# Kernel tuning notes

Measured on AMD Instinct MI355X. Metric: run time of the kernel, lower is better.

The kernel has to match this reference:

```python
import jax, jax.numpy as jnp
import numpy as np
from jax import lax

TOP_K = 2

def setup_inputs() -> dict:
    key = jax.random.key(0)
    ks = jax.random.split(key, 7)
    B, D, H, E = 8192, 1024, 4096, 8
    s = 0.02
    return {
        "x": jax.random.normal(ks[0], (B, D), jnp.float32),
        "wg": jax.random.normal(ks[1], (E, D), jnp.float32) * s,
        "bg": jnp.zeros((E,), jnp.float32),
        "w1": jax.random.normal(ks[2], (E, D, H), jnp.float32) * s,
        "b1": jnp.zeros((E, H), jnp.float32),
        "w2": jax.random.normal(ks[3], (E, H, D), jnp.float32) * s,
        "b2": jnp.zeros((E, D), jnp.float32),
    }

def reference(x, wg, bg, w1, b1, w2, b2):
    # Router: top-k logits, softmax over the selected k logits (TopKGate).
    logits = x @ wg.T + bg                      # (B, E)
    top_vals, top_idx = lax.top_k(logits, TOP_K)  # (B, K)
    gates = jax.nn.softmax(top_vals, axis=-1)     # (B, K)
    # Expert MLPs computed densely for all experts (vectorized reference;
    # dropout is identity in eval mode).
    h = jax.nn.relu(jnp.einsum('bd,edh->ebh', x, w1) + b1[:, None, :])  # (E, B, H)
    all_out = jnp.einsum('ebh,ehd->ebd', h, w2) + b2[:, None, :]        # (E, B, D)
    # Combine: gather each token's top-k expert outputs, weight by gates.
    per_tok = jnp.transpose(all_out, (1, 0, 2))                          # (B, E, D)
    sel = jnp.take_along_axis(per_tok, top_idx[:, :, None], axis=1)      # (B, K, D)
    return jnp.sum(sel * gates[:, :, None], axis=1)                      # (B, D)
```

## Files before the change

kernel.cpp:

```cpp
#include <hip/hip_runtime.h>
#include <hip/hip_bf16.h>
#include <math.h>

#define B_TOK 8192
#define D_DIM 1024
#define H_DIM 4096
#define E_NUM 8
#define NPAIR (B_TOK * 2)

typedef __bf16 bf16x8 __attribute__((ext_vector_type(8)));
typedef float f32x4 __attribute__((ext_vector_type(4)));
typedef unsigned short us4 __attribute__((ext_vector_type(4)));
typedef unsigned short us8 __attribute__((ext_vector_type(8)));

__device__ __forceinline__ unsigned short f2bf(float f) {
  union { float f; unsigned u; } v; v.f = f;
  unsigned r = v.u + 0x7FFFu + ((v.u >> 16) & 1u);
  return (unsigned short)(r >> 16);
}

__device__ __forceinline__ void gload16(const void* g, void* l) {
  __builtin_amdgcn_global_load_lds(
      (const __attribute__((address_space(1))) void*)g,
      (__attribute__((address_space(3))) void*)l, 16, 0, 0);
}

#define BARRIER()    asm volatile("s_barrier" ::: "memory")
#define VM4          asm volatile("s_waitcnt vmcnt(4)" ::: "memory")
#define VM0          asm volatile("s_waitcnt vmcnt(0)" ::: "memory")
#define LGKM0        asm volatile("s_waitcnt lgkmcnt(0)" ::: "memory")
#define RF(x) __builtin_amdgcn_readfirstlane(x)

__global__ void k_prep(const float* __restrict__ x, unsigned short* __restrict__ xb,
                       const float* __restrict__ w1, const float* __restrict__ w2,
                       unsigned short* __restrict__ w1t, unsigned short* __restrict__ w2t,
                       const float* __restrict__ wg, const float* __restrict__ bg,
                       int* __restrict__ tidx, float* __restrict__ tgate) {
  __shared__ unsigned short tl[64][68];
  int b = blockIdx.x;
  int tid = threadIdx.x;
  if (b < 2048) {
    int wid = tid >> 6, lane = tid & 63;
    int tok = b * 4 + wid;
    float acc[E_NUM];
#pragma unroll
    for (int e = 0; e < E_NUM; e++) acc[e] = 0.f;
    const float* xr = x + (size_t)tok * D_DIM;
#pragma unroll
    for (int it = 0; it < D_DIM / 256; it++) {
      int i = it * 256 + lane * 4;
      float4 xv = *(const float4*)(xr + i);
#pragma unroll
      for (int e = 0; e < E_NUM; e++) {
        float4 wv = *(const float4*)(wg + e * D_DIM + i);
        acc[e] += xv.x * wv.x + xv.y * wv.y + xv.z * wv.z + xv.w * wv.w;
      }
    }
#pragma unroll
    for (int e = 0; e < E_NUM; e++) {
#pragma unroll
      for (int off = 32; off; off >>= 1) acc[e] += __shfl_xor(acc[e], off);
    }
    if (lane == 0) {
      float v[E_NUM];
#pragma unroll
      for (int e = 0; e < E_NUM; e++) v[e] = acc[e] + bg[e];
      int i0 = 0; float v0 = v[0];
#pragma unroll
      for (int e = 1; e < E_NUM; e++) if (v[e] > v0) { v0 = v[e]; i0 = e; }
      int i1 = -1; float v1 = -1e30f;
#pragma unroll
      for (int e = 0; e < E_NUM; e++) if (e != i0 && v[e] > v1) { v1 = v[e]; i1 = e; }
      float g0 = 1.f / (1.f + expf(v1 - v0));
      float g1 = 1.f - g0;
      tidx[2 * tok] = i0; tidx[2 * tok + 1] = i1;
      tgate[2 * tok] = g0; tgate[2 * tok + 1] = g1;
    }
  } else if (b < 10240) {
    int i = ((b - 2048) * 256 + tid) * 4;
    float4 v = *(const float4*)(x + i);
    us4 o;
    o[0] = f2bf(v.x); o[1] = f2bf(v.y); o[2] = f2bf(v.z); o[3] = f2bf(v.w);
    *(us4*)(xb + i) = o;
  } else {
    int lb = b - 10240;
    int which = lb >> 13;
    int rem = lb & 8191;
    int e = rem >> 10;
    int local = rem & 1023;
    int R = which ? H_DIM : D_DIM;
    int C = which ? D_DIM : H_DIM;
    int CT = C >> 6;
    int ct = local & (CT - 1);
    int rt = local / CT;
    const float* ine = (which ? w2 : w1) + (size_t)e * D_DIM * H_DIM;
    unsigned short* oute = (which ? w2t : w1t) + (size_t)e * D_DIM * H_DIM;
    int r0 = rt * 64, c0 = ct * 64;
    int c4 = tid & 15, rg = tid >> 4;
    float4 v[4];
#pragma unroll
    for (int it = 0; it < 4; ++it)
      v[it] = *(const float4*)&ine[(size_t)(r0 + rg * 4 + it) * C + c0 + c4 * 4];
#pragma unroll
    for (int j = 0; j < 4; ++j) {
      us4 o;
      o[0] = f2bf(((const float*)&v[0])[j]);
      o[1] = f2bf(((const float*)&v[1])[j]);
      o[2] = f2bf(((const float*)&v[2])[j]);
      o[3] = f2bf(((const float*)&v[3])[j]);
      *(us4*)&tl[c4 * 4 + j][rg * 4] = o;
    }
    __syncthreads();
    int c = tid >> 2, g = tid & 3;
    us4 a0 = *(const us4*)&tl[c][g * 16 + 0];
    us4 a1 = *(const us4*)&tl[c][g * 16 + 4];
    us4 a2 = *(const us4*)&tl[c][g * 16 + 8];
    us4 a3 = *(const us4*)&tl[c][g * 16 + 12];
    us8 o0 = {a0[0], a0[1], a0[2], a0[3], a1[0], a1[1], a1[2], a1[3]};
    us8 o1 = {a2[0], a2[1], a2[2], a2[3], a3[0], a3[1], a3[2], a3[3]};
    size_t obase = (size_t)(c0 + c) * R + r0 + g * 16;
    *(us8*)&oute[obase] = o0;
    *(us8*)&oute[obase + 8] = o1;
  }
}

__global__ void k_count(const int* __restrict__ tidx, int* __restrict__ cnt) {
  __shared__ int lcnt[E_NUM];
  int tid = threadIdx.x;
  if (tid < E_NUM) lcnt[tid] = 0;
  __syncthreads();
  int t = blockIdx.x * 256 + tid;
  atomicAdd(&lcnt[tidx[2 * t]], 1);
  atomicAdd(&lcnt[tidx[2 * t + 1]], 1);
  __syncthreads();
  if (tid < E_NUM) atomicAdd(&cnt[tid], lcnt[tid]);
}

__global__ void k_prefix(int* __restrict__ meta) {
  if (threadIdx.x == 0) {
    int* cnt = meta;
    int* eoff = meta + 8;
    int* cursor = meta + 17;
    int* toff1 = meta + 25;
    int* toff2 = meta + 34;
    int a = 0, t1 = 0, t2 = 0;
    for (int e = 0; e < E_NUM; e++) {
      eoff[e] = a; cursor[e] = a; a += cnt[e];
      toff1[e] = t1; toff2[e] = t2;
      int mc = (cnt[e] + 127) >> 7;
      t1 += mc * (H_DIM / 128);
      t2 += mc * (D_DIM / 128);
    }
    eoff[E_NUM] = a; toff1[E_NUM] = t1; toff2[E_NUM] = t2;
  }
}

__global__ void k_scatter(const int* __restrict__ tidx, const float* __restrict__ tgate,
                          int* __restrict__ cursor, int* __restrict__ ptok,
                          float* __restrict__ pgate) {
  __shared__ int lcnt[E_NUM];
  __shared__ int base[E_NUM];
  int tid = threadIdx.x;
  if (tid < E_NUM) lcnt[tid] = 0;
  __syncthreads();
  int t = blockIdx.x * 256 + tid;
  int e0 = tidx[2 * t], e1 = tidx[2 * t + 1];
  int l0 = atomicAdd(&lcnt[e0], 1);
  int l1 = atomicAdd(&lcnt[e1], 1);
  __syncthreads();
  if (tid < E_NUM) base[tid] = atomicAdd(&cursor[tid], lcnt[tid]);
  __syncthreads();
  int p0 = base[e0] + l0;
  int p1 = base[e1] + l1;
  ptok[p0] = t; pgate[p0] = tgate[2 * t];
  ptok[p1] = t; pgate[p1] = tgate[2 * t + 1];
}

template <int KDIM, int NDIM, int MODE>
__global__ __launch_bounds__(256, 3) void k_gemm(
    const unsigned short* __restrict__ A, const unsigned short* __restrict__ Bt,
    const float* __restrict__ bias, const int* __restrict__ meta,
    const int* __restrict__ ptok, const float* __restrict__ pgate,
    unsigned short* __restrict__ Hout, float* __restrict__ Out) {
  constexpr int NT = NDIM / 128;
  constexpr int NKT = KDIM / 32;
  static_assert(NKT % 3 == 2 && NKT >= 8, "tail pattern requires NKT==2 mod 3");
  const int* eoff = meta + 8;
  const int* toff = (MODE == 1) ? (meta + 25) : (meta + 34);

  int tf[E_NUM + 1];
#pragma unroll
  for (int q = 0; q <= E_NUM; q++) tf[q] = RF(toff[q]);

  int nwg = gridDim.x;
  int bid = blockIdx.x;
  int i = (bid & 7) * (nwg >> 3) + (bid >> 3);
  if (i >= tf[E_NUM]) return;
  int e = 0;
#pragma unroll
  for (int q = 1; q < E_NUM; q++) e += (i >= tf[q]);
  int r = i - tf[e];
  int mt = r / NT;
  int nt = r - mt * NT;
  int off = RF(eoff[e]);
  int cnt = RF(eoff[e + 1]) - off;
  int m0 = mt * 128;

  __shared__ unsigned short lds[3][2][128 * 32];

  int tid = threadIdx.x;
  int w = tid >> 6, lane = tid & 63;
  int wm = w >> 1, wn = w & 1;

  int sseg = (lane & 3) ^ ((lane >> 3) & 3);
  const unsigned short* aSrc[2];
  const unsigned short* bSrc[2];
#pragma unroll
  for (int c = 0; c < 2; c++) {
    int q = w * 2 + c;
    int lrow = q * 16 + (lane >> 2);
    int arow = m0 + lrow;
    int ar = (arow < cnt) ? arow : (cnt - 1);
    size_t grow;
    if (MODE == 1) grow = (size_t)ptok[off + ar];
    else grow = (size_t)(off + ar);
    aSrc[c] = A + grow * KDIM + sseg * 8;
    int nrow = nt * 128 + q * 16 + (lane >> 2);
    bSrc[c] = Bt + (size_t)e * NDIM * KDIM + (size_t)nrow * KDIM + sseg * 8;
  }

  int segp = (lane >> 4) ^ ((lane >> 1) & 3);
  f32x4 acc[4][4] = {};

#define STAGE(buf, k0)                                          \
  {                                                             \
    _Pragma("unroll")                                           \
    for (int c = 0; c < 2; c++) {                               \
      int q = w * 2 + c;                                        \
      gload16(aSrc[c] + (k0), &lds[buf][0][q * 512]);           \
      gload16(bSrc[c] + (k0), &lds[buf][1][q * 512]);           \
    }                                                           \
  }
#define NOSTG ((void)0)

#define STEP(buf, WAITC, STGC)                                              \
  {                                                                         \
    WAITC; BARRIER();                                                       \
    STGC;                                                                   \
    bf16x8 aF[4], bF[4];                                                    \
    _Pragma("unroll")                                                       \
    for (int m = 0; m < 4; m++) {                                           \
      int row = wm * 64 + m * 16 + (lane & 15);                             \
      aF[m] = *(const bf16x8*)&lds[buf][0][row * 32 + segp * 8];            \
    }                                                                       \
    _Pragma("unroll")                                                       \
    for (int n = 0; n < 4; n++) {                                           \
      int row = wn * 64 + n * 16 + (lane & 15);                             \
      bF[n] = *(const bf16x8*)&lds[buf][1][row * 32 + segp * 8];            \
    }                                                                       \
    LGKM0;                                                                  \
    __builtin_amdgcn_s_setprio(1);                                          \
    _Pragma("unroll")                                                       \
    for (int m = 0; m < 4; m++)                                             \
      _Pragma("unroll")                                                     \
      for (int n = 0; n < 4; n++)                                           \
        acc[m][n] =                                                         \
            __builtin_amdgcn_mfma_f32_16x16x32_bf16(aF[m], bF[n], acc[m][n], 0, 0, 0); \
    __builtin_amdgcn_s_setprio(0);                                          \
  }

  STAGE(0, 0);
  STAGE(1, 32);

#pragma unroll 1
  for (int kt = 0; kt < NKT - 5; kt += 3) {
    STEP(0, VM4, STAGE(2, (kt + 2) * 32));
    STEP(1, VM4, STAGE(0, (kt + 3) * 32));
    STEP(2, VM4, STAGE(1, (kt + 4) * 32));
  }
  STEP(0, VM4, STAGE(2, (NKT - 3) * 32));
  STEP(1, VM4, STAGE(0, (NKT - 2) * 32));
  STEP(2, VM4, STAGE(1, (NKT - 1) * 32));
  STEP(0, VM4, NOSTG);
  STEP(1, VM0, NOSTG);

#undef STAGE
#undef NOSTG
#undef STEP

#pragma unroll
  for (int m = 0; m < 4; m++) {
    int lrowb = wm * 64 + m * 16 + (lane >> 4) * 4;
#pragma unroll
    for (int r2 = 0; r2 < 4; r2++) {
      int arow = m0 + lrowb + r2;
      if (arow < cnt) {
        if constexpr (MODE == 1) {
          size_t rowbase = (size_t)(off + arow) * NDIM;
#pragma unroll
          for (int n = 0; n < 4; n++) {
            int col = nt * 128 + wn * 64 + n * 16 + (lane & 15);
            float v = acc[m][n][r2] + bias[e * NDIM + col];
            v = v > 0.f ? v : 0.f;
            Hout[rowbase + col] = f2bf(v);
          }
        } else {
          int tok = ptok[off + arow];
          float g = pgate[off + arow];
#pragma unroll
          for (int n = 0; n < 4; n++) {
            int col = nt * 128 + wn * 64 + n * 16 + (lane & 15);
            float v = (acc[m][n][r2] + bias[e * NDIM + col]) * g;
            atomicAdd(Out + (size_t)tok * D_DIM + col, v);
          }
        }
      }
    }
  }
}

extern "C" void kernel_launch(void* const* d_in, const int* in_sizes, int n_in,
                              void* d_out, int out_size, void* d_ws, size_t ws_size,
                              hipStream_t stream) {
  const float* x  = (const float*)d_in[0];
  const float* wg = (const float*)d_in[1];
  const float* bg = (const float*)d_in[2];
  const float* w1 = (const float*)d_in[3];
  const float* b1 = (const float*)d_in[4];
  const float* w2 = (const float*)d_in[5];
  const float* b2 = (const float*)d_in[6];
  float* out = (float*)d_out;

  char* ws = (char*)d_ws;
  unsigned short* xb = (unsigned short*)ws;   ws += (size_t)B_TOK * D_DIM * 2;
  unsigned short* w1t = (unsigned short*)ws;  ws += (size_t)E_NUM * D_DIM * H_DIM * 2;
  unsigned short* w2t = (unsigned short*)ws;  ws += (size_t)E_NUM * D_DIM * H_DIM * 2;
  unsigned short* Hbuf = (unsigned short*)ws; ws += (size_t)NPAIR * H_DIM * 2;
  int* tidx = (int*)ws;    ws += (size_t)NPAIR * 4;
  float* tgate = (float*)ws; ws += (size_t)NPAIR * 4;
  int* ptok = (int*)ws;    ws += (size_t)NPAIR * 4;
  float* pgate = (float*)ws; ws += (size_t)NPAIR * 4;
  int* meta = (int*)ws;
  int* cnt = meta;
  int* cursor = meta + 17;

  hipMemsetAsync(meta, 0, 64 * sizeof(int), stream);
  hipMemsetAsync(out, 0, (size_t)out_size * sizeof(float), stream);

  k_prep<<<2048 + 8192 + 16384, 256, 0, stream>>>(
      x, xb, w1, w2, w1t, w2t, wg, bg, tidx, tgate);
  k_count<<<B_TOK / 256, 256, 0, stream>>>(tidx, cnt);
  k_prefix<<<1, 64, 0, stream>>>(meta);
  k_scatter<<<B_TOK / 256, 256, 0, stream>>>(tidx, tgate, cursor, ptok, pgate);
  k_gemm<D_DIM, H_DIM, 1><<<(NPAIR / 128 + E_NUM) * (H_DIM / 128), 256, 0, stream>>>(
      xb, w1t, b1, meta, ptok, pgate, Hbuf, nullptr);
  k_gemm<H_DIM, D_DIM, 2><<<(NPAIR / 128 + E_NUM) * (D_DIM / 128), 256, 0, stream>>>(
      Hbuf, w2t, b2, meta, ptok, pgate, nullptr, out);
}
```

Before: 580.7 us.

## Enlarge grouped GEMM M-tile from 128 to 192 rows per workgroup

Both expert GEMMs now use 192x128 output tiles, so each wave computes 96x64 with a 6x4 MFMA accumulator grid. The A-side LDS staging grows to three 16-row chunks per wave, and the wait counts are adjusted to five loads in flight. The prefix tile counts and the launch grid size change to match. This raises the reuse of each weight (B) tile and cuts the total number of tiles. The cost is more registers and LDS per workgroup, with occupancy lowered to 2 per SIMD, and more padding waste in the last tile of each expert.

```diff
diff --git a/kernel.cpp b/kernel.cpp
--- a/kernel.cpp
+++ b/kernel.cpp
@@ -7,6 +7,7 @@
 #define H_DIM 4096
 #define E_NUM 8
 #define NPAIR (B_TOK * 2)
+#define MT_WORST 93
 
 typedef __bf16 bf16x8 __attribute__((ext_vector_type(8)));
 typedef float f32x4 __attribute__((ext_vector_type(4)));
@@ -26,7 +27,7 @@
 }
 
 #define BARRIER()    asm volatile("s_barrier" ::: "memory")
-#define VM4          asm volatile("s_waitcnt vmcnt(4)" ::: "memory")
+#define VM5          asm volatile("s_waitcnt vmcnt(5)" ::: "memory")
 #define VM0          asm volatile("s_waitcnt vmcnt(0)" ::: "memory")
 #define LGKM0        asm volatile("s_waitcnt lgkmcnt(0)" ::: "memory")
 #define RF(x) __builtin_amdgcn_readfirstlane(x)
@@ -147,7 +148,7 @@
     for (int e = 0; e < E_NUM; e++) {
       eoff[e] = a; cursor[e] = a; a += cnt[e];
       toff1[e] = t1; toff2[e] = t2;
-      int mc = (cnt[e] + 127) >> 7;
+      int mc = (cnt[e] + 191) / 192;
       t1 += mc * (H_DIM / 128);
       t2 += mc * (D_DIM / 128);
     }
@@ -177,7 +178,7 @@
 }
 
 template <int KDIM, int NDIM, int MODE>
-__global__ __launch_bounds__(256, 3) void k_gemm(
+__global__ __launch_bounds__(256, 2) void k_gemm(
     const unsigned short* __restrict__ A, const unsigned short* __restrict__ Bt,
     const float* __restrict__ bias, const int* __restrict__ meta,
     const int* __restrict__ ptok, const float* __restrict__ pgate,
@@ -204,42 +205,45 @@
   int nt = r - mt * NT;
   int off = RF(eoff[e]);
   int cnt = RF(eoff[e + 1]) - off;
-  int m0 = mt * 128;
-
-  __shared__ unsigned short lds[3][2][128 * 32];
+  int m0 = mt * 192;
+
+  __shared__ unsigned short lds[3][6144 + 4096];
 
   int tid = threadIdx.x;
   int w = tid >> 6, lane = tid & 63;
   int wm = w >> 1, wn = w & 1;
 
   int sseg = (lane & 3) ^ ((lane >> 3) & 3);
-  const unsigned short* aSrc[2];
+  const unsigned short* aSrc[3];
   const unsigned short* bSrc[2];
 #pragma unroll
-  for (int c = 0; c < 2; c++) {
-    int q = w * 2 + c;
-    int lrow = q * 16 + (lane >> 2);
-    int arow = m0 + lrow;
+  for (int c = 0; c < 3; c++) {
+    int q = w * 3 + c;
+    int arow = m0 + q * 16 + (lane >> 2);
     int ar = (arow < cnt) ? arow : (cnt - 1);
     size_t grow;
     if (MODE == 1) grow = (size_t)ptok[off + ar];
     else grow = (size_t)(off + ar);
     aSrc[c] = A + grow * KDIM + sseg * 8;
+  }
+#pragma unroll
+  for (int c = 0; c < 2; c++) {
+    int q = w * 2 + c;
     int nrow = nt * 128 + q * 16 + (lane >> 2);
     bSrc[c] = Bt + (size_t)e * NDIM * KDIM + (size_t)nrow * KDIM + sseg * 8;
   }
 
   int segp = (lane >> 4) ^ ((lane >> 1) & 3);
-  f32x4 acc[4][4] = {};
-
-#define STAGE(buf, k0)                                          \
-  {                                                             \
-    _Pragma("unroll")                                           \
-    for (int c = 0; c < 2; c++) {                               \
-      int q = w * 2 + c;                                        \
-      gload16(aSrc[c] + (k0), &lds[buf][0][q * 512]);           \
-      gload16(bSrc[c] + (k0), &lds[buf][1][q * 512]);           \
-    }                                                           \
+  f32x4 acc[6][4] = {};
+
+#define STAGE(buf, k0)                                              \
+  {                                                                 \
+    _Pragma("unroll")                                               \
+    for (int c = 0; c < 3; c++)                                     \
+      gload16(aSrc[c] + (k0), &lds[buf][(w * 3 + c) * 512]);        \
+    _Pragma("unroll")                                               \
+    for (int c = 0; c < 2; c++)                                     \
+      gload16(bSrc[c] + (k0), &lds[buf][6144 + (w * 2 + c) * 512]); \
   }
 #define NOSTG ((void)0)
 
@@ -247,21 +251,21 @@
   {                                                                         \
     WAITC; BARRIER();                                                       \
     STGC;                                                                   \
-    bf16x8 aF[4], bF[4];                                                    \
+    bf16x8 aF[6], bF[4];                                                    \
     _Pragma("unroll")                                                       \
-    for (int m = 0; m < 4; m++) {                                           \
-      int row = wm * 64 + m * 16 + (lane & 15);                             \
-      aF[m] = *(const bf16x8*)&lds[buf][0][row * 32 + segp * 8];            \
+    for (int m = 0; m < 6; m++) {                                           \
+      int row = wm * 96 + m * 16 + (lane & 15);                             \
+      aF[m] = *(const bf16x8*)&lds[buf][row * 32 + segp * 8];               \
     }                                                                       \
     _Pragma("unroll")                                                       \
     for (int n = 0; n < 4; n++) {                                           \
       int row = wn * 64 + n * 16 + (lane & 15);                             \
-      bF[n] = *(const bf16x8*)&lds[buf][1][row * 32 + segp * 8];            \
+      bF[n] = *(const bf16x8*)&lds[buf][6144 + row * 32 + segp * 8];        \
     }                                                                       \
     LGKM0;                                                                  \
     __builtin_amdgcn_s_setprio(1);                                          \
     _Pragma("unroll")                                                       \
-    for (int m = 0; m < 4; m++)                                             \
+    for (int m = 0; m < 6; m++)                                             \
       _Pragma("unroll")                                                     \
       for (int n = 0; n < 4; n++)                                           \
         acc[m][n] =                                                         \
@@ -274,14 +278,14 @@
 
 #pragma unroll 1
   for (int kt = 0; kt < NKT - 5; kt += 3) {
-    STEP(0, VM4, STAGE(2, (kt + 2) * 32));
-    STEP(1, VM4, STAGE(0, (kt + 3) * 32));
-    STEP(2, VM4, STAGE(1, (kt + 4) * 32));
-  }
-  STEP(0, VM4, STAGE(2, (NKT - 3) * 32));
-  STEP(1, VM4, STAGE(0, (NKT - 2) * 32));
-  STEP(2, VM4, STAGE(1, (NKT - 1) * 32));
-  STEP(0, VM4, NOSTG);
+    STEP(0, VM5, STAGE(2, (kt + 2) * 32));
+    STEP(1, VM5, STAGE(0, (kt + 3) * 32));
+    STEP(2, VM5, STAGE(1, (kt + 4) * 32));
+  }
+  STEP(0, VM5, STAGE(2, (NKT - 3) * 32));
+  STEP(1, VM5, STAGE(0, (NKT - 2) * 32));
+  STEP(2, VM5, STAGE(1, (NKT - 1) * 32));
+  STEP(0, VM5, NOSTG);
   STEP(1, VM0, NOSTG);
 
 #undef STAGE
@@ -289,8 +293,8 @@
 #undef STEP
 
 #pragma unroll
-  for (int m = 0; m < 4; m++) {
-    int lrowb = wm * 64 + m * 16 + (lane >> 4) * 4;
+  for (int m = 0; m < 6; m++) {
+    int lrowb = wm * 96 + m * 16 + (lane >> 4) * 4;
 #pragma unroll
     for (int r2 = 0; r2 < 4; r2++) {
       int arow = m0 + lrowb + r2;
@@ -352,8 +356,8 @@
   k_count<<<B_TOK / 256, 256, 0, stream>>>(tidx, cnt);
   k_prefix<<<1, 64, 0, stream>>>(meta);
   k_scatter<<<B_TOK / 256, 256, 0, stream>>>(tidx, tgate, cursor, ptok, pgate);
-  k_gemm<D_DIM, H_DIM, 1><<<(NPAIR / 128 + E_NUM) * (H_DIM / 128), 256, 0, stream>>>(
+  k_gemm<D_DIM, H_DIM, 1><<<MT_WORST * (H_DIM / 128), 256, 0, stream>>>(
       xb, w1t, b1, meta, ptok, pgate, Hbuf, nullptr);
-  k_gemm<H_DIM, D_DIM, 2><<<(NPAIR / 128 + E_NUM) * (D_DIM / 128), 256, 0, stream>>>(
+  k_gemm<H_DIM, D_DIM, 2><<<MT_WORST * (D_DIM / 128), 256, 0, stream>>>(
       Hbuf, w2t, b2, meta, ptok, pgate, nullptr, out);
 }
```

After: 563.9 us (median of 2 runs). -2.9%, faster.
